# Performance work log

Measured on AMD Instinct MI355X. Metric: run time of the kernel, lower is better.

Reference implementation:

```python
import math
import jax, jax.numpy as jnp
import numpy as np

B, S, D, H, DH, R, V = 8, 1024, 1024, 8, 512, 36, 32002  # DH = d_model//2, HD = h*DH = 4096
HD = H * DH
LN_EPS = 1e-5


def setup_inputs() -> dict:
    key = jax.random.key(0)
    ks = jax.random.split(key, 16)

    def n(k, shp, std=0.02):
        return jax.random.normal(k, shp, jnp.float32) * std

    pre_words = jax.random.randint(ks[0], (B, S), 0, V)
    img_features = jax.random.normal(ks[1], (B, R, D), jnp.float32)
    exp_embed = n(ks[2], (V, D)).at[0].set(0.0)  # padding_idx=0
    # id2visual table: sparse nonneg rows over 36 regions; zero rows -> textual tokens
    id2vis = (jax.random.uniform(ks[3], (V, R)) < 0.05).astype(jnp.float32)
    # stacked params for 2 transformer layers; weights stored (in, out) so y = x @ W + b
    wq = n(ks[4], (2, D, HD)); bq = jnp.zeros((2, HD), jnp.float32)
    wk = n(ks[5], (2, D, HD)); bk = jnp.zeros((2, HD), jnp.float32)
    wv = n(ks[6], (2, D, HD)); bv = jnp.zeros((2, HD), jnp.float32)
    wo = n(ks[7], (2, HD, D)); bo = jnp.zeros((2, D), jnp.float32)
    w1 = n(ks[8], (2, D, D)); b1 = jnp.zeros((2, D), jnp.float32)
    w2 = n(ks[9], (2, D, D)); b2 = jnp.zeros((2, D), jnp.float32)
    ln1_g = jnp.ones((2, D), jnp.float32); ln1_b = jnp.zeros((2, D), jnp.float32)
    ln2_g = jnp.ones((2, D), jnp.float32); ln2_b = jnp.zeros((2, D), jnp.float32)
    return dict(pre_words=pre_words, img_features=img_features, exp_embed=exp_embed,
                id2vis=id2vis, wq=wq, bq=bq, wk=wk, bk=bk, wv=wv, bv=bv, wo=wo, bo=bo,
                w1=w1, b1=b1, w2=w2, b2=b2, ln1_g=ln1_g, ln1_b=ln1_b, ln2_g=ln2_g, ln2_b=ln2_b)


def _layer_norm(x, g, b):
    m = x.mean(-1, keepdims=True)
    v = ((x - m) ** 2).mean(-1, keepdims=True)
    return (x - m) / jnp.sqrt(v + LN_EPS) * g + b


def _softmax_one(x):
    # shifted-denominator softmax: exp(x - max) / (1 + sum exp(x - max))
    x = x - x.max(-1, keepdims=True)
    e = jnp.exp(x)
    return e / (1.0 + e.sum(-1, keepdims=True))


def reference(pre_words, img_features, exp_embed, id2vis, wq, bq, wk, bk, wv, bv,
              wo, bo, w1, b1, w2, b2, ln1_g, ln1_b, ln2_g, ln2_b):
    # token embedding: textual (masked to 0 where a visual row exists) + visual bmm
    te = exp_embed[pre_words]                       # (B,S,D)
    vids = id2vis[pre_words]                        # (B,S,R)
    word_mask = vids.sum(-1, keepdims=True) != 0    # (B,S,1)
    ve = jnp.einsum('bsr,brd->bsd', vids, img_features)
    x = jnp.where(word_mask, 0.0, te) + ve          # (B,S,D)

    scale = 1.0 / math.sqrt(DH)
    for i in range(2):  # two structurally identical transformer layers
        h = _layer_norm(x, ln1_g[i], ln1_b[i])
        q = (h @ wq[i] + bq[i]).reshape(B, S, H, DH).transpose(0, 2, 1, 3)
        k = (h @ wk[i] + bk[i]).reshape(B, S, H, DH).transpose(0, 2, 1, 3)
        v = (h @ wv[i] + bv[i]).reshape(B, S, H, DH).transpose(0, 2, 1, 3)
        attn = _softmax_one(jnp.einsum('bhqd,bhkd->bhqk', q, k) * scale)  # (B,H,S,S)
        o = jnp.einsum('bhqk,bhkd->bhqd', attn, v)
        o = o.transpose(0, 2, 1, 3).reshape(B, S, HD)
        x = x + (o @ wo[i] + bo[i])
        f = _layer_norm(x, ln2_g[i], ln2_b[i])
        f = jax.nn.gelu(f @ w1[i] + b1[i], approximate=False) @ w2[i] + b2[i]
        x = x + f
    return x
```

## Files before the change

### kernel.cpp

```cpp
#include <hip/hip_runtime.h>


using u16 = unsigned short;
typedef __attribute__((ext_vector_type(8))) short bf16x8;
typedef __attribute__((ext_vector_type(4))) float f32x4;

__device__ __forceinline__ float b2f(u16 u) {
  union { unsigned int i; float f; } v; v.i = ((unsigned int)u) << 16; return v.f;
}
__device__ __forceinline__ u16 f2b(float f) {
  union { float f; unsigned int i; } v; v.f = f;
  unsigned int i = v.i;
  return (u16)((i + 0x7FFFu + ((i >> 16) & 1u)) >> 16);
}
__device__ __forceinline__ float gelu_f(float x) {
  return 0.5f * x * (1.f + erff(x * 0.70710678118654752f));
}
__device__ __forceinline__ void async16(void* lds, const void* g) {
  __builtin_amdgcn_global_load_lds((const __attribute__((address_space(1))) void*)g,
                                   (__attribute__((address_space(3))) void*)lds, 16, 0, 0);
}
__device__ __forceinline__ void storeC(float* p, float v) { *p = v; }
__device__ __forceinline__ void storeC(u16* p, float v) { *p = f2b(v); }

__global__ __launch_bounds__(256) void embed_k(
    const int* __restrict__ words, const float* __restrict__ img,
    const float* __restrict__ emb, const float* __restrict__ id2v,
    float* __restrict__ x)
{
  __shared__ float vs[36];
  int tok = blockIdx.x, b = tok >> 10, t = threadIdx.x;
  int wd = words[tok];
  if (t < 36) vs[t] = id2v[(size_t)wd * 36 + t];
  __syncthreads();
  bool any = false;
#pragma unroll
  for (int r = 0; r < 36; ++r) any = any || (vs[r] != 0.f);
#pragma unroll
  for (int i = 0; i < 4; ++i) {
    int d = t + (i << 8);
    float acc = 0.f;
    for (int r = 0; r < 36; ++r) {
      float vv = vs[r];
      if (vv != 0.f) acc += vv * img[((size_t)(b * 36 + r) << 10) + d];
    }
    float te = any ? 0.f : emb[((size_t)wd << 10) + d];
    x[((size_t)tok << 10) + d] = te + acc;
  }
}

__global__ __launch_bounds__(256) void ln_k(
    const float* __restrict__ x, u16* __restrict__ out,
    const float* __restrict__ g, const float* __restrict__ bb)
{
  __shared__ float red[4];
  int row = blockIdx.x, t = threadIdx.x;
  const float* xr = x + ((size_t)row << 10);
  float v[4], s = 0.f;
#pragma unroll
  for (int i = 0; i < 4; ++i) { v[i] = xr[t + (i << 8)]; s += v[i]; }
#pragma unroll
  for (int o = 32; o; o >>= 1) s += __shfl_xor(s, o, 64);
  if ((t & 63) == 0) red[t >> 6] = s;
  __syncthreads();
  s = red[0] + red[1] + red[2] + red[3];
  float mean = s * 0.0009765625f;
  float q = 0.f;
#pragma unroll
  for (int i = 0; i < 4; ++i) { float d = v[i] - mean; q += d * d; }
  __syncthreads();
#pragma unroll
  for (int o = 32; o; o >>= 1) q += __shfl_xor(q, o, 64);
  if ((t & 63) == 0) red[t >> 6] = q;
  __syncthreads();
  q = red[0] + red[1] + red[2] + red[3];
  float rstd = rsqrtf(q * 0.0009765625f + 1e-5f);
  u16* orow = out + ((size_t)row << 10);
#pragma unroll
  for (int i = 0; i < 4; ++i) {
    int d = t + (i << 8);
    orow[d] = f2b((v[i] - mean) * rstd * g[d] + bb[d]);
  }
}

__global__ __launch_bounds__(256) void sm_k(const u16* __restrict__ S, u16* __restrict__ P)
{
  __shared__ float red[4];
  size_t row = blockIdx.x;
  int t = threadIdx.x;
  const u16* sr = S + (row << 10);
  ushort4 sv = *(const ushort4*)(sr + (t << 2));
  float v[4] = { b2f(sv.x), b2f(sv.y), b2f(sv.z), b2f(sv.w) };
  float m = fmaxf(fmaxf(v[0], v[1]), fmaxf(v[2], v[3]));
#pragma unroll
  for (int o = 32; o; o >>= 1) m = fmaxf(m, __shfl_xor(m, o, 64));
  if ((t & 63) == 0) red[t >> 6] = m;
  __syncthreads();
  m = fmaxf(fmaxf(red[0], red[1]), fmaxf(red[2], red[3]));
  float e[4], s = 0.f;
#pragma unroll
  for (int i = 0; i < 4; ++i) { e[i] = __expf(v[i] - m); s += e[i]; }
  __syncthreads();
#pragma unroll
  for (int o = 32; o; o >>= 1) s += __shfl_xor(s, o, 64);
  if ((t & 63) == 0) red[t >> 6] = s;
  __syncthreads();
  s = red[0] + red[1] + red[2] + red[3];
  float inv = 1.f / (1.f + s);
  ushort4 pv;
  pv.x = f2b(e[0] * inv); pv.y = f2b(e[1] * inv);
  pv.z = f2b(e[2] * inv); pv.w = f2b(e[3] * inv);
  *(ushort4*)(P + (row << 10) + (t << 2)) = pv;
}

__global__ __launch_bounds__(256) void tr_k(
    const float* __restrict__ src, u16* __restrict__ dst, int ls, int ld)
{
  __shared__ u16 tile[64][65];
  int c0 = blockIdx.x << 6, r0 = blockIdx.y << 6;
  int tx = threadIdx.x & 63, ty0 = threadIdx.x >> 6;
#pragma unroll
  for (int i = 0; i < 16; ++i) {
    int ty = (ty0 << 4) + i;
    tile[ty][tx] = f2b(src[(size_t)(r0 + ty) * ls + (c0 + tx)]);
  }
  __syncthreads();
#pragma unroll
  for (int i = 0; i < 16; ++i) {
    int ty = (ty0 << 4) + i;
    dst[(size_t)(c0 + ty) * ld + (r0 + tx)] = tile[tx][ty];
  }
}

template <typename CT, int ACT, int BIAS, int RESID, int BN>
__global__ __launch_bounds__(256, 4) void gemm_t(
    const u16* __restrict__ A, const u16* __restrict__ Bt,
    CT* __restrict__ C, const float* __restrict__ bias,
    const float* __restrict__ resid,
    int M, int N, int K, int lda, int ldb, int ldc, float scale,
    int zbase, int zdiv, int ga, int gb, int gc,
    long long aS1, long long aS2, long long bS1, long long bS2,
    long long cS1, long long cS2)
{
  constexpr int NACC = BN / 32;
  __shared__ u16 lA[128 * 64];
  __shared__ u16 lB[BN * 64];
  const int nwg = gridDim.x * gridDim.y;
  const int id = blockIdx.y * gridDim.x + blockIdx.x;
  const int qq = nwg >> 3, rr8 = nwg & 7;
  const int xcd = id & 7, off = id >> 3;
  const int swz = (xcd < rr8 ? xcd * (qq + 1) : rr8 * (qq + 1) + (xcd - rr8) * qq) + off;
  const int bx = swz % gridDim.x, by = swz / gridDim.x;

  long long lz = blockIdx.z;
  long long gz = zbase + lz;
  long long zA = ga ? gz : lz, zB = gb ? gz : lz, zC = gc ? gz : lz;
  size_t aOff = (size_t)((zA / zdiv) * aS1 + (zA % zdiv) * aS2);
  size_t bOff = (size_t)((zB / zdiv) * bS1 + (zB % zdiv) * bS2);
  size_t cOff = (size_t)((zC / zdiv) * cS1 + (zC % zdiv) * cS2);
  const int m0 = by << 7, n0 = bx * BN;
  const int tid = threadIdx.x, lane = tid & 63, w = tid >> 6;
  const int wm = w >> 1, wn = w & 1;
  const int srow8 = lane >> 3;
  const int schunk = (lane & 7) ^ srow8;
  const int fr = lane & 15, hi = lane >> 4;

  f32x4 acc[4][NACC];
#pragma unroll
  for (int mi = 0; mi < 4; ++mi)
#pragma unroll
    for (int ni = 0; ni < NACC; ++ni) acc[mi][ni] = 0.f;

  const u16* Ab = A + aOff;
  const u16* Bb = Bt + bOff;

  for (int k0 = 0; k0 < K; k0 += 64) {
#pragma unroll
    for (int s = 0; s < 4; ++s) {
      const int rb = (s << 5) + (w << 3);
      async16(&lA[rb << 6], Ab + (size_t)(m0 + rb + srow8) * lda + (k0 + (schunk << 3)));
    }
#pragma unroll
    for (int s = 0; s < BN / 32; ++s) {
      const int rb = (s << 5) + (w << 3);
      async16(&lB[rb << 6], Bb + (size_t)(n0 + rb + srow8) * ldb + (k0 + (schunk << 3)));
    }
    __syncthreads();
#pragma unroll
    for (int ks = 0; ks < 2; ++ks) {
      const int q = (ks << 2) + hi;
      bf16x8 a8[4], b8[NACC];
#pragma unroll
      for (int mi = 0; mi < 4; ++mi) {
        const int R = (wm << 6) + (mi << 4) + fr;
        a8[mi] = *(const bf16x8*)&lA[(R << 6) + ((q ^ (R & 7)) << 3)];
      }
#pragma unroll
      for (int ni = 0; ni < NACC; ++ni) {
        const int R = wn * (BN / 2) + (ni << 4) + fr;
        b8[ni] = *(const bf16x8*)&lB[(R << 6) + ((q ^ (R & 7)) << 3)];
      }
#pragma unroll
      for (int mi = 0; mi < 4; ++mi)
#pragma unroll
        for (int ni = 0; ni < NACC; ++ni)
          acc[mi][ni] = __builtin_amdgcn_mfma_f32_16x16x32_bf16(a8[mi], b8[ni], acc[mi][ni], 0, 0, 0);
    }
    __syncthreads();
  }

  const int r4 = hi << 2, cc = fr;
#pragma unroll
  for (int mi = 0; mi < 4; ++mi) {
#pragma unroll
    for (int ni = 0; ni < NACC; ++ni) {
      const int col = n0 + wn * (BN / 2) + (ni << 4) + cc;
      float bcol = 0.f;
      if (BIAS == 1) bcol = bias[col];
#pragma unroll
      for (int j = 0; j < 4; ++j) {
        const int row = m0 + (wm << 6) + (mi << 4) + r4 + j;
        float v = acc[mi][ni][j] * scale + bcol;
        if (BIAS == 2) v += bias[row];
        if (ACT == 1) v = gelu_f(v);
        const size_t idx = cOff + (size_t)row * ldc + col;
        if (RESID) v += resid[idx];
        storeC(&C[idx], v);
      }
    }
  }
}

extern "C" void kernel_launch(void* const* d_in, const int* in_sizes, int n_in,
                              void* d_out, int out_size, void* d_ws, size_t ws_size,
                              hipStream_t stream)
{
  (void)in_sizes; (void)n_in; (void)out_size;
  const int*   pre_words = (const int*)d_in[0];
  const float* img  = (const float*)d_in[1];
  const float* emb  = (const float*)d_in[2];
  const float* id2v = (const float*)d_in[3];
  const float* wq = (const float*)d_in[4];  const float* bq = (const float*)d_in[5];
  const float* wk = (const float*)d_in[6];  const float* bk = (const float*)d_in[7];
  const float* wv = (const float*)d_in[8];  const float* bv = (const float*)d_in[9];
  const float* wo = (const float*)d_in[10]; const float* bo = (const float*)d_in[11];
  const float* w1 = (const float*)d_in[12]; const float* b1 = (const float*)d_in[13];
  const float* w2 = (const float*)d_in[14]; const float* b2 = (const float*)d_in[15];
  const float* ln1g = (const float*)d_in[16]; const float* ln1b = (const float*)d_in[17];
  const float* ln2g = (const float*)d_in[18]; const float* ln2b = (const float*)d_in[19];

  const size_t FIXED = 88080384 + (size_t)(1 << 16);
  int g = 1;
  for (int c = 8; c >= 1; c >>= 1)
    if (FIXED + (size_t)c * 33554432 + 4194304 <= ws_size) { g = c; break; }
  int nc = 1;
  int ncmax = 8 * g > 32 ? 32 : 8 * g;
  for (int c = ncmax; c >= 1; c >>= 1)
    if (FIXED + (size_t)g * 33554432 + (size_t)c * 4194304 <= ws_size) { nc = c; break; }

  char* p = (char*)d_ws;
  auto alloc = [&](size_t bytes) -> void* {
    void* r = (void*)p; p += (bytes + 255) & ~(size_t)255; return r;
  };
  float* x  = (float*)alloc((size_t)8192 * 1024 * 4);
  u16* h    = (u16*)alloc((size_t)8192 * 1024 * 2);
  u16* Qg   = (u16*)alloc((size_t)g * 1024 * 4096 * 2);
  u16* Og   = (u16*)alloc((size_t)g * 1024 * 4096 * 2);
  u16* ff   = Qg;
  u16* Kg   = (u16*)alloc((size_t)g * 1024 * 4096 * 2);
  u16* Vtg  = (u16*)alloc((size_t)g * 4096 * 1024 * 2);
  u16* wqt  = (u16*)alloc((size_t)4096 * 1024 * 2);
  u16* wkt  = (u16*)alloc((size_t)4096 * 1024 * 2);
  u16* wvt  = (u16*)alloc((size_t)4096 * 1024 * 2);
  u16* wot  = (u16*)alloc((size_t)1024 * 4096 * 2);
  u16* w1t  = (u16*)alloc((size_t)1024 * 1024 * 2);
  u16* w2t  = (u16*)alloc((size_t)1024 * 1024 * 2);
  u16* Sc   = (u16*)alloc((size_t)nc << 21);
  u16* Pp   = (u16*)alloc((size_t)nc << 21);

  embed_k<<<8192, 256, 0, stream>>>(pre_words, img, emb, id2v, x);

  const float qk_scale = 0.044194173824159216f;
  for (int L = 0; L < 2; ++L) {
    const float* WQ = wq + (size_t)L * 1024 * 4096;
    const float* WK = wk + (size_t)L * 1024 * 4096;
    const float* WV = wv + (size_t)L * 1024 * 4096;
    const float* WO = wo + (size_t)L * 4096 * 1024;
    const float* W1 = w1 + (size_t)L * 1024 * 1024;
    const float* W2 = w2 + (size_t)L * 1024 * 1024;

    tr_k<<<dim3(64, 16), 256, 0, stream>>>(WQ, wqt, 4096, 1024);
    tr_k<<<dim3(64, 16), 256, 0, stream>>>(WK, wkt, 4096, 1024);
    tr_k<<<dim3(64, 16), 256, 0, stream>>>(WV, wvt, 4096, 1024);
    tr_k<<<dim3(16, 64), 256, 0, stream>>>(WO, wot, 1024, 4096);
    tr_k<<<dim3(16, 16), 256, 0, stream>>>(W1, w1t, 1024, 1024);
    tr_k<<<dim3(16, 16), 256, 0, stream>>>(W2, w2t, 1024, 1024);

    ln_k<<<8192, 256, 0, stream>>>(x, h, ln1g + L * 1024, ln1b + L * 1024);

    for (int g0 = 0; g0 < 8; g0 += g) {
      const u16* hg = h + (size_t)g0 * 1048576;
      const int Mg = 1024 * g;
      gemm_t<u16, 0, 1, 0, 128><<<dim3(32, Mg >> 7), 256, 0, stream>>>(
          hg, wqt, Qg, bq + (size_t)L * 4096, nullptr,
          Mg, 4096, 1024, 1024, 1024, 4096, 1.f,
          0, 1, 0, 0, 0, 0, 0, 0, 0, 0, 0);
      gemm_t<u16, 0, 1, 0, 128><<<dim3(32, Mg >> 7), 256, 0, stream>>>(
          hg, wkt, Kg, bk + (size_t)L * 4096, nullptr,
          Mg, 4096, 1024, 1024, 1024, 4096, 1.f,
          0, 1, 0, 0, 0, 0, 0, 0, 0, 0, 0);
      gemm_t<u16, 0, 2, 0, 128><<<dim3(8, 32, g), 256, 0, stream>>>(
          wvt, h, Vtg, bv + (size_t)L * 4096, nullptr,
          4096, 1024, 1024, 1024, 1024, 1024, 1.f,
          g0, 1, 0, 1, 0, 0, 0, 1048576LL, 0, 4194304LL, 0);
      for (int c0 = 0; c0 < 8 * g; c0 += nc) {
        gemm_t<u16, 0, 0, 0, 128><<<dim3(8, 8, nc), 256, 0, stream>>>(
            Qg, Kg, Sc, nullptr, nullptr,
            1024, 1024, 512, 4096, 4096, 1024, qk_scale,
            c0, 8, 1, 1, 0,
            4194304LL, 512LL, 4194304LL, 512LL, 8388608LL, 1048576LL);
        sm_k<<<nc << 10, 256, 0, stream>>>(Sc, Pp);
        gemm_t<u16, 0, 0, 0, 128><<<dim3(4, 8, nc), 256, 0, stream>>>(
            Pp, Vtg, Og, nullptr, nullptr,
            1024, 512, 1024, 1024, 1024, 4096, 1.f,
            c0, 8, 0, 1, 1,
            8388608LL, 1048576LL, 4194304LL, 524288LL, 4194304LL, 512LL);
      }
      gemm_t<float, 0, 1, 1, 64><<<dim3(16, Mg >> 7), 256, 0, stream>>>(
          Og, wot, x + (size_t)g0 * 1048576, bo + (size_t)L * 1024,
          x + (size_t)g0 * 1048576,
          Mg, 1024, 4096, 4096, 4096, 1024, 1.f,
          0, 1, 0, 0, 0, 0, 0, 0, 0, 0, 0);
    }

    ln_k<<<8192, 256, 0, stream>>>(x, h, ln2g + L * 1024, ln2b + L * 1024);

    gemm_t<u16, 1, 1, 0, 64><<<dim3(16, 64), 256, 0, stream>>>(
        h, w1t, ff, b1 + (size_t)L * 1024, nullptr,
        8192, 1024, 1024, 1024, 1024, 1024, 1.f,
        0, 1, 0, 0, 0, 0, 0, 0, 0, 0, 0);
    float* cdst = (L == 1) ? (float*)d_out : x;
    gemm_t<float, 0, 1, 1, 64><<<dim3(16, 64), 256, 0, stream>>>(
        ff, w2t, cdst, b2 + (size_t)L * 1024, x,
        8192, 1024, 1024, 1024, 1024, 1024, 1.f,
        0, 1, 0, 0, 0, 0, 0, 0, 0, 0, 0);
  }
}
```

Before: 1.524 ms.

## Add 256x256-tile double-buffered 8-wave GEMM for QKV and attention matmuls

Adds a new GEMM kernel with 256x256 output tiles, 512 threads (8 waves, 2x4), async global-to-LDS double buffering with swizzled LDS layout and XCD-aware block remapping. It replaces the 128-tile kernel for the Q/K/V projections and the QK^T and PV batched matmuls. Larger tiles raise arithmetic intensity and cut global traffic per FLOP, and prefetching two stages ahead overlaps loads with MFMA. In exchange it uses 128KB of LDS and many accumulator registers, so occupancy drops to one block per CU, and some grids become small (e.g. 2x4xnc for PV), which risks underfilling the GPU.

```diff
diff --git a/kernel.cpp b/kernel.cpp
--- a/kernel.cpp
+++ b/kernel.cpp
@@ -129,6 +129,117 @@
   for (int i = 0; i < 16; ++i) {
     int ty = (ty0 << 4) + i;
     dst[(size_t)(c0 + ty) * ld + (r0 + tx)] = tile[tx][ty];
+  }
+}
+
+template <typename CT, int ACT, int BIAS, int RESID>
+__global__ __launch_bounds__(512, 1) void gemm8p(
+    const u16* __restrict__ A, const u16* __restrict__ Bt,
+    CT* __restrict__ C, const float* __restrict__ bias,
+    const float* __restrict__ resid,
+    int M, int N, int K, int lda, int ldb, int ldc, float scale,
+    int zbase, int zdiv, int ga, int gb, int gc,
+    long long aS1, long long aS2, long long bS1, long long bS2,
+    long long cS1, long long cS2)
+{
+  __shared__ u16 lA[2][256 * 64];
+  __shared__ u16 lB[2][256 * 64];
+  const int nwg = gridDim.x * gridDim.y;
+  const int id = blockIdx.y * gridDim.x + blockIdx.x;
+  const int qq = nwg >> 3, rr8 = nwg & 7;
+  const int xcd = id & 7, off = id >> 3;
+  const int swz = (xcd < rr8 ? xcd * (qq + 1) : rr8 * (qq + 1) + (xcd - rr8) * qq) + off;
+  const int bx = swz % gridDim.x, by = swz / gridDim.x;
+
+  long long lz = blockIdx.z;
+  long long gz = zbase + lz;
+  long long zA = ga ? gz : lz, zB = gb ? gz : lz, zC = gc ? gz : lz;
+  size_t aOff = (size_t)((zA / zdiv) * aS1 + (zA % zdiv) * aS2);
+  size_t bOff = (size_t)((zB / zdiv) * bS1 + (zB % zdiv) * bS2);
+  size_t cOff = (size_t)((zC / zdiv) * cS1 + (zC % zdiv) * cS2);
+  const int m0 = by << 8, n0 = bx << 8;
+  const int tid = threadIdx.x, lane = tid & 63, w = tid >> 6;
+  const int wm = w >> 2, wn = w & 3;
+  const int srow8 = lane >> 3;
+  const int schunk = (lane & 7) ^ srow8;
+  const int fr = lane & 15, hi = lane >> 4;
+
+  f32x4 acc[8][4];
+#pragma unroll
+  for (int mi = 0; mi < 8; ++mi)
+#pragma unroll
+    for (int ni = 0; ni < 4; ++ni) acc[mi][ni] = 0.f;
+
+  const u16* Ab = A + aOff;
+  const u16* Bb = Bt + bOff;
+
+  auto STAGE = [&](int buf, int k0) {
+#pragma unroll
+    for (int s = 0; s < 4; ++s) {
+      const int rb = (s << 6) + (w << 3);
+      async16(&lA[buf][rb << 6], Ab + (size_t)(m0 + rb + srow8) * lda + (k0 + (schunk << 3)));
+      async16(&lB[buf][rb << 6], Bb + (size_t)(n0 + rb + srow8) * ldb + (k0 + (schunk << 3)));
+    }
+  };
+
+  const int nt = K >> 6;
+  STAGE(0, 0);
+  STAGE(1, 64);
+  for (int t = 0; t < nt; ++t) {
+    const int cur = t & 1;
+    if (t + 1 < nt) asm volatile("s_waitcnt vmcnt(8)" ::: "memory");
+    else            asm volatile("s_waitcnt vmcnt(0)" ::: "memory");
+    __builtin_amdgcn_s_barrier();
+    __builtin_amdgcn_sched_barrier(0);
+#pragma unroll
+    for (int ks = 0; ks < 2; ++ks) {
+      const int q = (ks << 2) + hi;
+      bf16x8 a8[8], b8[4];
+#pragma unroll
+      for (int mi = 0; mi < 8; ++mi) {
+        const int R = (wm << 7) + (mi << 4) + fr;
+        a8[mi] = *(const bf16x8*)&lA[cur][(R << 6) + ((q ^ (R & 7)) << 3)];
+      }
+#pragma unroll
+      for (int ni = 0; ni < 4; ++ni) {
+        const int R = (wn << 6) + (ni << 4) + fr;
+        b8[ni] = *(const bf16x8*)&lB[cur][(R << 6) + ((q ^ (R & 7)) << 3)];
+      }
+      __builtin_amdgcn_s_setprio(1);
+#pragma unroll
+      for (int mi = 0; mi < 8; ++mi)
+#pragma unroll
+        for (int ni = 0; ni < 4; ++ni)
+          acc[mi][ni] = __builtin_amdgcn_mfma_f32_16x16x32_bf16(a8[mi], b8[ni], acc[mi][ni], 0, 0, 0);
+      __builtin_amdgcn_s_setprio(0);
+    }
+    if (t + 2 < nt) {
+      asm volatile("s_waitcnt lgkmcnt(0)" ::: "memory");
+      __builtin_amdgcn_s_barrier();
+      __builtin_amdgcn_sched_barrier(0);
+      STAGE(cur, (t + 2) << 6);
+    }
+  }
+
+  const int r4 = hi << 2, cc = fr;
+#pragma unroll
+  for (int mi = 0; mi < 8; ++mi) {
+#pragma unroll
+    for (int ni = 0; ni < 4; ++ni) {
+      const int col = n0 + (wn << 6) + (ni << 4) + cc;
+      float bcol = 0.f;
+      if (BIAS == 1) bcol = bias[col];
+#pragma unroll
+      for (int j = 0; j < 4; ++j) {
+        const int row = m0 + (wm << 7) + (mi << 4) + r4 + j;
+        float v = acc[mi][ni][j] * scale + bcol;
+        if (BIAS == 2) v += bias[row];
+        if (ACT == 1) v = gelu_f(v);
+        const size_t idx = cOff + (size_t)row * ldc + col;
+        if (RESID) v += resid[idx];
+        storeC(&C[idx], v);
+      }
+    }
   }
 }
 
@@ -301,26 +412,26 @@
     for (int g0 = 0; g0 < 8; g0 += g) {
       const u16* hg = h + (size_t)g0 * 1048576;
       const int Mg = 1024 * g;
-      gemm_t<u16, 0, 1, 0, 128><<<dim3(32, Mg >> 7), 256, 0, stream>>>(
+      gemm8p<u16, 0, 1, 0><<<dim3(16, Mg >> 8), 512, 0, stream>>>(
           hg, wqt, Qg, bq + (size_t)L * 4096, nullptr,
           Mg, 4096, 1024, 1024, 1024, 4096, 1.f,
           0, 1, 0, 0, 0, 0, 0, 0, 0, 0, 0);
-      gemm_t<u16, 0, 1, 0, 128><<<dim3(32, Mg >> 7), 256, 0, stream>>>(
+      gemm8p<u16, 0, 1, 0><<<dim3(16, Mg >> 8), 512, 0, stream>>>(
           hg, wkt, Kg, bk + (size_t)L * 4096, nullptr,
           Mg, 4096, 1024, 1024, 1024, 4096, 1.f,
           0, 1, 0, 0, 0, 0, 0, 0, 0, 0, 0);
-      gemm_t<u16, 0, 2, 0, 128><<<dim3(8, 32, g), 256, 0, stream>>>(
+      gemm8p<u16, 0, 2, 0><<<dim3(4, 16, g), 512, 0, stream>>>(
           wvt, h, Vtg, bv + (size_t)L * 4096, nullptr,
           4096, 1024, 1024, 1024, 1024, 1024, 1.f,
           g0, 1, 0, 1, 0, 0, 0, 1048576LL, 0, 4194304LL, 0);
       for (int c0 = 0; c0 < 8 * g; c0 += nc) {
-        gemm_t<u16, 0, 0, 0, 128><<<dim3(8, 8, nc), 256, 0, stream>>>(
+        gemm8p<u16, 0, 0, 0><<<dim3(4, 4, nc), 512, 0, stream>>>(
             Qg, Kg, Sc, nullptr, nullptr,
             1024, 1024, 512, 4096, 4096, 1024, qk_scale,
             c0, 8, 1, 1, 0,
             4194304LL, 512LL, 4194304LL, 512LL, 8388608LL, 1048576LL);
         sm_k<<<nc << 10, 256, 0, stream>>>(Sc, Pp);
-        gemm_t<u16, 0, 0, 0, 128><<<dim3(4, 8, nc), 256, 0, stream>>>(
+        gemm8p<u16, 0, 0, 0><<<dim3(2, 4, nc), 512, 0, stream>>>(
             Pp, Vtg, Og, nullptr, nullptr,
             1024, 512, 1024, 1024, 1024, 4096, 1.f,
             c0, 8, 0, 1, 1,
```

New measurement: 1.496 ms. Within noise of the previous version (-1.9%).
